# Performance work log

Hardware: AMD Instinct MI355X
Metric: run time of the kernel (lower is better)

Reference implementation:

```python
import jax, jax.numpy as jnp
import numpy as np

D = 512
B = 128
V = 1024
MAX_LEN = 5000


def _pos_encoding(d, max_len):
    # sinusoidal PE table [max_len, d], identical to the torch buffer
    pos = np.arange(max_len, dtype=np.float32)[:, None]
    div = np.exp(np.arange(0, d, 2, dtype=np.float32) * (-np.log(10000.0) / d))
    pe = np.zeros((max_len, d), dtype=np.float32)
    pe[:, 0::2] = np.sin(pos * div)
    pe[:, 1::2] = np.cos(pos * div)
    return jnp.asarray(pe)


def setup_inputs() -> dict:
    key = jax.random.key(0)
    ks = jax.random.split(key, 16)
    s = 0.02  # weight scale
    return {
        "x": jax.random.normal(ks[0], (B, V), jnp.float32),
        "timesteps": jax.random.randint(ks[1], (B,), 0, 1000),
        "query_emb": jax.random.normal(ks[2], (B, D), jnp.float32),
        "target_emb": jax.random.normal(ks[3], (B, V, D), jnp.float32),
        "Wq": jax.random.normal(ks[4], (D, D), jnp.float32) * s,
        "Wk": jax.random.normal(ks[5], (D, D), jnp.float32) * s,
        "Wv": jax.random.normal(ks[6], (D, D), jnp.float32) * s,
        "Wp": jax.random.normal(ks[7], (D, D), jnp.float32) * s,
        "bp": jnp.zeros((D,), jnp.float32),
        "Wt1": jax.random.normal(ks[8], (D, D), jnp.float32) * s,
        "bt1": jnp.zeros((D,), jnp.float32),
        "Wt2": jax.random.normal(ks[9], (D, D), jnp.float32) * s,
        "bt2": jnp.zeros((D,), jnp.float32),
        "Wd1": jax.random.normal(ks[10], (2 * D, 2 * D), jnp.float32) * s,
        "bd1": jnp.zeros((2 * D,), jnp.float32),
        "Wd2": jax.random.normal(ks[11], (1, 2 * D), jnp.float32) * s,
        "bd2": jnp.zeros((1,), jnp.float32),
    }


def reference(x, timesteps, query_emb, target_emb,
              Wq, Wk, Wv, Wp, bp, Wt1, bt1, Wt2, bt2,
              Wd1, bd1, Wd2, bd2):
    pe = _pos_encoding(D, MAX_LEN)
    # timestep embedding: pe[t] -> SiLU MLP  (dropout in eval mode = identity)
    t = pe[timesteps]                                      # [B, D]
    cond = jax.nn.silu(t @ Wt1.T + bt1) @ Wt2.T + bt2      # [B, D]
    q = (query_emb + cond) @ Wq.T                          # [B, D]
    tc = target_emb + cond[:, None, :]                     # [B, V, D]
    k = tc @ Wk.T
    v = tc @ Wv.T
    # single-query attention with additive bias x
    weight = jax.nn.softmax(jnp.einsum('bd,bvd->bv', q, k) + x, axis=-1)  # [B, V]
    new_emb = jnp.einsum('bv,bvd->bd', weight, v) @ Wp.T + bp             # [B, D]
    # concat-MLP decoder over all candidates
    emb = jnp.concatenate(
        [jnp.broadcast_to(new_emb[:, None, :], target_emb.shape), target_emb],
        axis=-1)                                            # [B, V, 2D]
    h = jax.nn.relu(emb @ Wd1.T + bd1)                      # [B, V, 2D]
    p = (h @ Wd2.T + bd2)[..., 0] + weight                  # [B, V]
    return p
```

## Files before the change

### kernel.cpp

```cpp
#include <hip/hip_runtime.h>
#include <hip/hip_bf16.h>


typedef __attribute__((ext_vector_type(8))) short bhalf8_t;
typedef __attribute__((ext_vector_type(8))) unsigned short ushort8_t;
typedef __attribute__((ext_vector_type(4))) float fx4_t;

__device__ __forceinline__ unsigned short f2bf(float f) {
  unsigned int u = __float_as_uint(f);
  unsigned int r = (u + 0x7FFFu + ((u >> 16) & 1u)) >> 16;
  return (unsigned short)r;
}
__device__ __forceinline__ float bf2f(unsigned short h) {
  return __uint_as_float((unsigned int)h << 16);
}

__device__ __forceinline__ float wave_sum64(float s) {
#pragma unroll
  for (int o = 32; o; o >>= 1) s += __shfl_xor(s, o, 64);
  return s;
}

__global__ __launch_bounds__(256) void transpose5_kernel(
    const float* __restrict__ s0, const float* __restrict__ s1, const float* __restrict__ s2,
    const float* __restrict__ s3, const float* __restrict__ s4,
    float* __restrict__ d0, float* __restrict__ d1, float* __restrict__ d2,
    float* __restrict__ d3, float* __restrict__ d4) {
  __shared__ float t[32][33];
  const float* src; float* dst;
  switch (blockIdx.z) {
    case 0: src = s0; dst = d0; break;
    case 1: src = s1; dst = d1; break;
    case 2: src = s2; dst = d2; break;
    case 3: src = s3; dst = d3; break;
    default: src = s4; dst = d4; break;
  }
  const int tx = threadIdx.x & 31, ty = threadIdx.x >> 5;
  const int c0 = blockIdx.x * 32, r0 = blockIdx.y * 32;
#pragma unroll
  for (int i = 0; i < 32; i += 8)
    t[ty + i][tx] = src[(size_t)(r0 + ty + i) * 512 + c0 + tx];
  __syncthreads();
#pragma unroll
  for (int i = 0; i < 32; i += 8)
    dst[(size_t)(c0 + ty + i) * 512 + r0 + tx] = t[tx][ty + i];
}

__global__ __launch_bounds__(256) void transposed1_kernel(const float* __restrict__ src,
                                                          float* __restrict__ dst) {
  __shared__ float t[32][33];
  const int tx = threadIdx.x & 31, ty = threadIdx.x >> 5;
  const int c0 = blockIdx.x * 32, r0 = blockIdx.y * 32;
#pragma unroll
  for (int i = 0; i < 32; i += 8)
    t[ty + i][tx] = src[(size_t)(r0 + ty + i) * 1024 + c0 + tx];
  __syncthreads();
#pragma unroll
  for (int i = 0; i < 32; i += 8)
    dst[(size_t)(c0 + ty + i) * 1024 + r0 + tx] = t[tx][ty + i];
}

template <int MODE, int ACT, int DOT>
__global__ __launch_bounds__(256) void gvec_kernel(
    const float* __restrict__ WT, int n, const float* __restrict__ src1,
    const float* __restrict__ src2, const float* __restrict__ bias,
    const int* __restrict__ timesteps, float* __restrict__ outp,
    float* __restrict__ dotout) {
  __shared__ __attribute__((aligned(16))) float arow[512];
  const int b = blockIdx.x, tid = threadIdx.x;
  if (MODE == 0) {
    const int ts = timesteps[b];
    const float NEG = -9.2103403719761836f / 512.f;
    float dv = expf((float)(2 * tid) * NEG);
    float ang = (float)ts * dv;
    arow[2 * tid] = sinf(ang);
    arow[2 * tid + 1] = cosf(ang);
  } else {
#pragma unroll
    for (int k = tid; k < 512; k += 256) {
      float a;
      if (MODE == 1) {
        a = src1[(size_t)b * 512 + k];
      } else if (MODE == 2) {
        a = src1[(size_t)b * 512 + k] + src2[(size_t)b * 512 + k];
      } else {
        a = src2[(size_t)b * 512 + k];
#pragma unroll
        for (int q = 0; q < 8; ++q) a += src1[((size_t)b * 8 + q) * 512 + k];
      }
      arow[k] = a;
    }
  }
  __syncthreads();
  const int j = blockIdx.y * 256 + tid;
  const float* w = WT + j;
  float s0 = 0.f, s1 = 0.f, s2 = 0.f, s3 = 0.f;
#pragma unroll 4
  for (int k = 0; k < 512; k += 4) {
    s0 = fmaf(arow[k], w[(size_t)k * n], s0);
    s1 = fmaf(arow[k + 1], w[(size_t)(k + 1) * n], s1);
    s2 = fmaf(arow[k + 2], w[(size_t)(k + 2) * n], s2);
    s3 = fmaf(arow[k + 3], w[(size_t)(k + 3) * n], s3);
  }
  float s = (s0 + s1) + (s2 + s3);
  if (bias) s += bias[j];
  if (ACT == 1) s = s / (1.f + expf(-s));
  outp[(size_t)b * n + j] = s;
  if (DOT) {
    float p = s * src2[(size_t)b * 512 + j];
    p = wave_sum64(p);
    __shared__ float rd[4];
    if ((tid & 63) == 0) rd[tid >> 6] = p;
    __syncthreads();
    if (tid == 0) atomicAdd(dotout + b, rd[0] + rd[1] + rd[2] + rd[3]);
  }
}

__global__ __launch_bounds__(256) void convw_kernel(const float* __restrict__ Wd1,
                                                    unsigned short* __restrict__ wsW) {
  const int g = blockIdx.x * 256 + threadIdx.x;
  const int lane = g & 63;
  const int kc = (g >> 6) & 1;
  const int nhn = (g >> 7) & 7;
  const int ks = (g >> 10) & 7;
  const int nc = g >> 13;
  const int j = nc * 128 + (nhn >> 1) * 32 + (nhn & 1) * 16 + (lane & 15);
  const int k = ks * 64 + kc * 32 + (lane >> 4) * 8;
  const float* src = Wd1 + (size_t)j * 1024 + 512 + k;
  float4 f0 = *(const float4*)src;
  float4 f1 = *(const float4*)(src + 4);
  ushort4 h0 = make_ushort4(f2bf(f0.x), f2bf(f0.y), f2bf(f0.z), f2bf(f0.w));
  ushort4 h1 = make_ushort4(f2bf(f1.x), f2bf(f1.y), f2bf(f1.z), f2bf(f1.w));
  ushort4* dst = (ushort4*)((char*)wsW + (size_t)g * 16);
  dst[0] = h0;
  dst[1] = h1;
}

__global__ __launch_bounds__(256) void logits_kernel(
    const float* __restrict__ te, const float* __restrict__ qk,
    const float* __restrict__ constb, const float* __restrict__ x,
    float* __restrict__ logits, unsigned short* __restrict__ te16, int w16) {
  const int wave = threadIdx.x >> 6, lane = threadIdx.x & 63;
  const size_t r = (size_t)blockIdx.x * 4 + wave;
  const int b = (int)(r >> 10);
  const float4* t4 = (const float4*)(te + r * 512);
  const float4* q4 = (const float4*)(qk + (size_t)b * 512);
  float4 a0 = t4[lane], a1 = t4[lane + 64];
  float4 c0 = q4[lane], c1 = q4[lane + 64];
  float s = a0.x * c0.x + a0.y * c0.y + a0.z * c0.z + a0.w * c0.w +
            a1.x * c1.x + a1.y * c1.y + a1.z * c1.z + a1.w * c1.w;
  s = wave_sum64(s);
  if (w16) {
    ushort4 h0 = make_ushort4(f2bf(a0.x), f2bf(a0.y), f2bf(a0.z), f2bf(a0.w));
    ushort4 h1 = make_ushort4(f2bf(a1.x), f2bf(a1.y), f2bf(a1.z), f2bf(a1.w));
    *(ushort4*)(te16 + r * 512 + lane * 4) = h0;
    *(ushort4*)(te16 + r * 512 + 256 + lane * 4) = h1;
  }
  if (lane == 0) logits[r] = s + constb[b] + x[r];
}

__global__ __launch_bounds__(256) void softmax_kernel(
    const float* __restrict__ logits, const float* __restrict__ bd2,
    float* __restrict__ weight, float* __restrict__ out) {
  __shared__ float sm[4];
  const int b = blockIdx.x, tid = threadIdx.x;
  const int wave = tid >> 6, lane = tid & 63;
  float4 l4 = ((const float4*)(logits + (size_t)b * 1024))[tid];
  float m = fmaxf(fmaxf(l4.x, l4.y), fmaxf(l4.z, l4.w));
#pragma unroll
  for (int o = 32; o; o >>= 1) m = fmaxf(m, __shfl_xor(m, o, 64));
  if (lane == 0) sm[wave] = m;
  __syncthreads();
  float M = fmaxf(fmaxf(sm[0], sm[1]), fmaxf(sm[2], sm[3]));
  __syncthreads();
  float e0 = expf(l4.x - M), e1 = expf(l4.y - M), e2 = expf(l4.z - M), e3 = expf(l4.w - M);
  float ssum = wave_sum64(e0 + e1 + e2 + e3);
  if (lane == 0) sm[wave] = ssum;
  __syncthreads();
  float inv = 1.f / (sm[0] + sm[1] + sm[2] + sm[3]);
  float c = bd2[0];
  float4 w4 = make_float4(e0 * inv, e1 * inv, e2 * inv, e3 * inv);
  ((float4*)(weight + (size_t)b * 1024))[tid] = w4;
  ((float4*)(out + (size_t)b * 1024))[tid] = make_float4(w4.x + c, w4.y + c, w4.z + c, w4.w + c);
}

__global__ __launch_bounds__(256) void wsum32_kernel(const float* __restrict__ te,
                                                     const float* __restrict__ weight,
                                                     float* __restrict__ spart) {
  __shared__ float wl[128];
  const int b = blockIdx.x >> 3, vq = blockIdx.x & 7;
  const int tid = threadIdx.x;
  if (tid < 128) wl[tid] = weight[(size_t)b * 1024 + vq * 128 + tid];
  __syncthreads();
  const float* tb = te + ((size_t)b * 1024 + (size_t)vq * 128) * 512;
  float s0 = 0.f, s1 = 0.f;
#pragma unroll 4
  for (int v = 0; v < 128; ++v) {
    float w = wl[v];
    s0 += w * tb[(size_t)v * 512 + tid];
    s1 += w * tb[(size_t)v * 512 + 256 + tid];
  }
  spart[(size_t)blockIdx.x * 512 + tid] = s0;
  spart[(size_t)blockIdx.x * 512 + 256 + tid] = s1;
}

__global__ __launch_bounds__(256) void wsum16_kernel(const unsigned short* __restrict__ te16,
                                                     const float* __restrict__ weight,
                                                     float* __restrict__ spart) {
  __shared__ float wl[128];
  __shared__ float red[4][512];
  const int b = blockIdx.x >> 3, vq = blockIdx.x & 7;
  const int tid = threadIdx.x;
  if (tid < 128) wl[tid] = weight[(size_t)b * 1024 + vq * 128 + tid];
  __syncthreads();
  const int g = tid & 63, vh = tid >> 6;
  const unsigned short* base =
      te16 + ((size_t)b * 1024 + vq * 128 + vh * 32) * 512 + g * 8;
  float acc[8] = {};
  for (int v = 0; v < 32; ++v) {
    float w = wl[vh * 32 + v];
    ushort8_t h = *(const ushort8_t*)(base + (size_t)v * 512);
#pragma unroll
    for (int i = 0; i < 8; ++i) acc[i] += w * bf2f(h[i]);
  }
#pragma unroll
  for (int i = 0; i < 8; ++i) red[vh][g * 8 + i] = acc[i];
  __syncthreads();
  for (int d = tid; d < 512; d += 256)
    spart[(size_t)blockIdx.x * 512 + d] =
        red[0][d] + red[1][d] + red[2][d] + red[3][d];
}

#define GLD16(g, l)                                                              \
  __builtin_amdgcn_global_load_lds((const __attribute__((address_space(1))) void*)(g), \
                                   (__attribute__((address_space(3))) void*)(l), 16, 0, 0)

template <int USE16>
__global__ __launch_bounds__(512, 2) void decoder_kernel(
    const float* __restrict__ te, const unsigned short* __restrict__ te16,
    const unsigned short* __restrict__ wsW, const float* __restrict__ A,
    const float* __restrict__ Wd2, float* __restrict__ out) {
  extern __shared__ char lds[];

  const int tid = threadIdx.x;
  const int wave = tid >> 6, lane = tid & 63;
  const int lhi = lane >> 4, llo = lane & 15;
  const int mh = wave >> 2, nh = wave & 3;
  const size_t row0 = (size_t)blockIdx.x * 64;
  const int b = (int)(blockIdx.x >> 4);

  bhalf8_t a[2][16];
  if (USE16) {
#pragma unroll
    for (int m = 0; m < 2; ++m) {
      const char* rowp = (const char*)te16 + (row0 + mh * 32 + m * 16 + llo) * 1024 + lhi * 16;
#pragma unroll
      for (int s = 0; s < 16; ++s) a[m][s] = *(const bhalf8_t*)(rowp + s * 64);
    }
  } else {
#pragma unroll
    for (int m = 0; m < 2; ++m) {
      const char* rowp = (const char*)te + (row0 + mh * 32 + m * 16 + llo) * 2048 + lhi * 32;
#pragma unroll
      for (int s = 0; s < 16; ++s) {
        float4 f0 = *(const float4*)(rowp + s * 128);
        float4 f1 = *(const float4*)(rowp + s * 128 + 16);
        bhalf8_t h;
        h[0] = (short)f2bf(f0.x); h[1] = (short)f2bf(f0.y);
        h[2] = (short)f2bf(f0.z); h[3] = (short)f2bf(f0.w);
        h[4] = (short)f2bf(f1.x); h[5] = (short)f2bf(f1.y);
        h[6] = (short)f2bf(f1.z); h[7] = (short)f2bf(f1.w);
        a[m][s] = h;
      }
    }
  }

  float av[8][2], wv[8][2];
#pragma unroll
  for (int nc = 0; nc < 8; ++nc) {
    const int jb = nc * 128 + nh * 32 + llo;
    av[nc][0] = A[(size_t)b * 1024 + jb];
    av[nc][1] = A[(size_t)b * 1024 + jb + 16];
    wv[nc][0] = Wd2[jb];
    wv[nc][1] = Wd2[jb + 16];
  }

#pragma unroll
  for (int m = 0; m < 2; ++m)
#pragma unroll
    for (int s = 0; s < 16; ++s) asm volatile("" : "+v"(a[m][s]));
#pragma unroll
  for (int nc = 0; nc < 8; ++nc)
    asm volatile("" : "+v"(av[nc][0]), "+v"(av[nc][1]), "+v"(wv[nc][0]), "+v"(wv[nc][1]));

  auto stage = [&](int c) {
    const char* src = (const char*)wsW + (size_t)c * 16384 + wave * 1024 + lane * 16;
    char* dst = lds + (c & 3) * 16384 + wave * 1024;
    GLD16(src, dst);
    GLD16(src + 8192, dst + 8192);
  };
  stage(0); stage(1); stage(2);

  fx4_t acc[2][2];
  const fx4_t zf = {0.f, 0.f, 0.f, 0.f};
  float pacc[2][4] = {};

#pragma unroll
  for (int nc = 0; nc < 8; ++nc) {
#pragma unroll
    for (int ks = 0; ks < 8; ++ks) {
      const int c = nc * 8 + ks;
      if (c <= 61)      asm volatile("s_waitcnt vmcnt(4)" ::: "memory");
      else if (c == 62) asm volatile("s_waitcnt vmcnt(2)" ::: "memory");
      else              asm volatile("s_waitcnt vmcnt(0)" ::: "memory");
      __builtin_amdgcn_s_barrier();
      __builtin_amdgcn_sched_barrier(0);
      if (ks == 0) { acc[0][0] = zf; acc[0][1] = zf; acc[1][0] = zf; acc[1][1] = zf; }
      const char* wb = lds + (c & 3) * 16384 + nh * 4096 + lane * 16;
      bhalf8_t b00 = *(const bhalf8_t*)(wb);
      bhalf8_t b01 = *(const bhalf8_t*)(wb + 1024);
      bhalf8_t b10 = *(const bhalf8_t*)(wb + 2048);
      bhalf8_t b11 = *(const bhalf8_t*)(wb + 3072);
      acc[0][0] = __builtin_amdgcn_mfma_f32_16x16x32_bf16(a[0][ks * 2 + 0], b00, acc[0][0], 0, 0, 0);
      acc[0][0] = __builtin_amdgcn_mfma_f32_16x16x32_bf16(a[0][ks * 2 + 1], b01, acc[0][0], 0, 0, 0);
      acc[0][1] = __builtin_amdgcn_mfma_f32_16x16x32_bf16(a[0][ks * 2 + 0], b10, acc[0][1], 0, 0, 0);
      acc[0][1] = __builtin_amdgcn_mfma_f32_16x16x32_bf16(a[0][ks * 2 + 1], b11, acc[0][1], 0, 0, 0);
      acc[1][0] = __builtin_amdgcn_mfma_f32_16x16x32_bf16(a[1][ks * 2 + 0], b00, acc[1][0], 0, 0, 0);
      acc[1][0] = __builtin_amdgcn_mfma_f32_16x16x32_bf16(a[1][ks * 2 + 1], b01, acc[1][0], 0, 0, 0);
      acc[1][1] = __builtin_amdgcn_mfma_f32_16x16x32_bf16(a[1][ks * 2 + 0], b10, acc[1][1], 0, 0, 0);
      acc[1][1] = __builtin_amdgcn_mfma_f32_16x16x32_bf16(a[1][ks * 2 + 1], b11, acc[1][1], 0, 0, 0);
      if (c <= 60) stage(c + 3);
      if (ks == 7) {
#pragma unroll
        for (int m = 0; m < 2; ++m)
#pragma unroll
          for (int rg = 0; rg < 4; ++rg)
            pacc[m][rg] += fmaxf(acc[m][0][rg] + av[nc][0], 0.f) * wv[nc][0] +
                           fmaxf(acc[m][1][rg] + av[nc][1], 0.f) * wv[nc][1];
      }
    }
  }

  __syncthreads();
  float* red = (float*)lds;
#pragma unroll
  for (int m = 0; m < 2; ++m)
#pragma unroll
    for (int rg = 0; rg < 4; ++rg) {
      float sv = pacc[m][rg];
      sv += __shfl_xor(sv, 1, 64);
      sv += __shfl_xor(sv, 2, 64);
      sv += __shfl_xor(sv, 4, 64);
      sv += __shfl_xor(sv, 8, 64);
      if (llo == 0) red[nh * 64 + mh * 32 + m * 16 + lhi * 4 + rg] = sv;
    }
  __syncthreads();
  if (tid < 64) {
    float s = red[tid] + red[64 + tid] + red[128 + tid] + red[192 + tid];
    out[row0 + tid] += s;
  }
}

extern "C" void kernel_launch(void* const* d_in, const int* in_sizes, int n_in,
                              void* d_out, int out_size, void* d_ws, size_t ws_size,
                              hipStream_t stream) {
  const float* x = (const float*)d_in[0];
  const int* tsteps = (const int*)d_in[1];
  const float* qe = (const float*)d_in[2];
  const float* te = (const float*)d_in[3];
  const float* Wq = (const float*)d_in[4];
  const float* Wk = (const float*)d_in[5];
  const float* Wv = (const float*)d_in[6];
  const float* Wp = (const float*)d_in[7];
  const float* bp = (const float*)d_in[8];
  const float* Wt1 = (const float*)d_in[9];
  const float* bt1 = (const float*)d_in[10];
  const float* Wt2 = (const float*)d_in[11];
  const float* bt2 = (const float*)d_in[12];
  const float* Wd1 = (const float*)d_in[13];
  const float* bd1 = (const float*)d_in[14];
  const float* Wd2 = (const float*)d_in[15];
  const float* bd2 = (const float*)d_in[16];
  float* out = (float*)d_out;

  char* ws = (char*)d_ws;
  unsigned short* wsW = (unsigned short*)(ws + 0);
  float* Wt1T = (float*)(ws + 1048576);
  float* Wt2T = (float*)(ws + 2097152);
  float* WqT = (float*)(ws + 3145728);
  float* WvT = (float*)(ws + 4194304);
  float* WpT = (float*)(ws + 5242880);
  float* Wd1aT = (float*)(ws + 6291456);
  float* cond = (float*)(ws + 8388608);
  float* qk = (float*)(ws + 8650752);
  float* hbuf = (float*)(ws + 8912896);
  float* qbuf = (float*)(ws + 9175040);
  float* ubuf = (float*)(ws + 9437184);
  float* nebuf = (float*)(ws + 9699328);
  float* cb = (float*)(ws + 9961472);
  float* logits = (float*)(ws + 9965568);
  float* wgt = (float*)(ws + 10489856);
  float* spart = (float*)(ws + 11014144);
  float* Abuf = (float*)(ws + 13111296);
  const size_t TE16_OFF = 14680064;
  const size_t TE16_BYTES = (size_t)128 * 1024 * 512 * 2;
  unsigned short* te16 = (unsigned short*)(ws + TE16_OFF);
  const int use16 = (ws_size >= TE16_OFF + TE16_BYTES) ? 1 : 0;

  transpose5_kernel<<<dim3(16, 16, 5), 256, 0, stream>>>(Wt1, Wt2, Wq, Wv, Wp,
                                                         Wt1T, Wt2T, WqT, WvT, WpT);
  transposed1_kernel<<<dim3(16, 32), 256, 0, stream>>>(Wd1, Wd1aT);
  convw_kernel<<<256, 256, 0, stream>>>(Wd1, wsW);

  hipMemsetAsync(cb, 0, 128 * sizeof(float), stream);
  gvec_kernel<0, 1, 0><<<dim3(128, 2), 256, 0, stream>>>(Wt1T, 512, nullptr, nullptr, bt1, tsteps, hbuf, nullptr);
  gvec_kernel<1, 0, 0><<<dim3(128, 2), 256, 0, stream>>>(Wt2T, 512, hbuf, nullptr, bt2, nullptr, cond, nullptr);
  gvec_kernel<2, 0, 0><<<dim3(128, 2), 256, 0, stream>>>(WqT, 512, qe, cond, nullptr, nullptr, qbuf, nullptr);
  gvec_kernel<1, 0, 1><<<dim3(128, 2), 256, 0, stream>>>(Wk, 512, qbuf, cond, nullptr, nullptr, qk, cb);

  logits_kernel<<<32768, 256, 0, stream>>>(te, qk, cb, x, logits, te16, use16);
  softmax_kernel<<<128, 256, 0, stream>>>(logits, bd2, wgt, out);
  if (use16)
    wsum16_kernel<<<1024, 256, 0, stream>>>(te16, wgt, spart);
  else
    wsum32_kernel<<<1024, 256, 0, stream>>>(te, wgt, spart);

  gvec_kernel<3, 0, 0><<<dim3(128, 2), 256, 0, stream>>>(WvT, 512, spart, cond, nullptr, nullptr, ubuf, nullptr);
  gvec_kernel<1, 0, 0><<<dim3(128, 2), 256, 0, stream>>>(WpT, 512, ubuf, nullptr, bp, nullptr, nebuf, nullptr);
  gvec_kernel<1, 0, 0><<<dim3(128, 4), 256, 0, stream>>>(Wd1aT, 1024, nebuf, nullptr, bd1, nullptr, Abuf, nullptr);

  if (use16) {
    (void)hipFuncSetAttribute((const void*)decoder_kernel<1>,
                              hipFuncAttributeMaxDynamicSharedMemorySize, 65536);
    decoder_kernel<1><<<2048, 512, 65536, stream>>>(te, te16, wsW, Abuf, Wd2, out);
  } else {
    (void)hipFuncSetAttribute((const void*)decoder_kernel<0>,
                              hipFuncAttributeMaxDynamicSharedMemorySize, 65536);
    decoder_kernel<0><<<2048, 512, 65536, stream>>>(te, te16, wsW, Abuf, Wd2, out);
  }
}
```

Baseline: 474.7 us.

## Fuse weight prep and small GEMV chains into few kernels, tweak decoder staging

Merges the transpose and bf16 conversion kernels into one prep launch, fuses the four front GEMVs (timestep MLP, q, qk, cb) into one per-batch kernel, and fuses the three back GEMVs into another. This removes a memset and many small launches along with their intermediate buffers. The decoder now starts weight staging before its A-operand loads, pins the A fragments in AGPRs, drops the occupancy hint from launch bounds, and moves the reduction scratch past a larger LDS allocation. Each fused kernel runs only 128 blocks, so the GEMVs get less parallelism, and the extra LDS may lower decoder occupancy.

```diff
diff --git a/kernel.cpp b/kernel.cpp
--- a/kernel.cpp
+++ b/kernel.cpp
@@ -21,119 +21,199 @@
   return s;
 }
 
-__global__ __launch_bounds__(256) void transpose5_kernel(
-    const float* __restrict__ s0, const float* __restrict__ s1, const float* __restrict__ s2,
-    const float* __restrict__ s3, const float* __restrict__ s4,
-    float* __restrict__ d0, float* __restrict__ d1, float* __restrict__ d2,
-    float* __restrict__ d3, float* __restrict__ d4) {
-  __shared__ float t[32][33];
-  const float* src; float* dst;
-  switch (blockIdx.z) {
-    case 0: src = s0; dst = d0; break;
-    case 1: src = s1; dst = d1; break;
-    case 2: src = s2; dst = d2; break;
-    case 3: src = s3; dst = d3; break;
-    default: src = s4; dst = d4; break;
-  }
-  const int tx = threadIdx.x & 31, ty = threadIdx.x >> 5;
-  const int c0 = blockIdx.x * 32, r0 = blockIdx.y * 32;
-#pragma unroll
-  for (int i = 0; i < 32; i += 8)
-    t[ty + i][tx] = src[(size_t)(r0 + ty + i) * 512 + c0 + tx];
-  __syncthreads();
-#pragma unroll
-  for (int i = 0; i < 32; i += 8)
-    dst[(size_t)(c0 + ty + i) * 512 + r0 + tx] = t[tx][ty + i];
-}
-
-__global__ __launch_bounds__(256) void transposed1_kernel(const float* __restrict__ src,
-                                                          float* __restrict__ dst) {
+__global__ __launch_bounds__(256) void prepw_kernel(
+    const float* __restrict__ Wt1, const float* __restrict__ Wt2, const float* __restrict__ Wq,
+    const float* __restrict__ Wv, const float* __restrict__ Wp, const float* __restrict__ Wd1,
+    float* __restrict__ Wt1T, float* __restrict__ Wt2T, float* __restrict__ WqT,
+    float* __restrict__ WvT, float* __restrict__ WpT, float* __restrict__ Wd1aT,
+    unsigned short* __restrict__ wsW) {
+  const int z = blockIdx.z;
+  if (z == 6) {
+    if (blockIdx.y >= 16) return;
+    const int g = (blockIdx.y * 16 + blockIdx.x) * 256 + threadIdx.x;
+    const int lane = g & 63;
+    const int kc = (g >> 6) & 1;
+    const int nhn = (g >> 7) & 7;
+    const int ks = (g >> 10) & 7;
+    const int nc = g >> 13;
+    const int j = nc * 128 + (nhn >> 1) * 32 + (nhn & 1) * 16 + (lane & 15);
+    const int k = ks * 64 + kc * 32 + (lane >> 4) * 8;
+    const float* src = Wd1 + (size_t)j * 1024 + 512 + k;
+    float4 f0 = *(const float4*)src;
+    float4 f1 = *(const float4*)(src + 4);
+    ushort4 h0 = make_ushort4(f2bf(f0.x), f2bf(f0.y), f2bf(f0.z), f2bf(f0.w));
+    ushort4 h1 = make_ushort4(f2bf(f1.x), f2bf(f1.y), f2bf(f1.z), f2bf(f1.w));
+    ushort4* dst = (ushort4*)((char*)wsW + (size_t)g * 16);
+    dst[0] = h0;
+    dst[1] = h1;
+    return;
+  }
   __shared__ float t[32][33];
   const int tx = threadIdx.x & 31, ty = threadIdx.x >> 5;
   const int c0 = blockIdx.x * 32, r0 = blockIdx.y * 32;
+  if (z == 5) {
+    const float* src = Wd1;
+    float* dst = Wd1aT;
+#pragma unroll
+    for (int i = 0; i < 32; i += 8)
+      t[ty + i][tx] = src[(size_t)(r0 + ty + i) * 1024 + c0 + tx];
+    __syncthreads();
+#pragma unroll
+    for (int i = 0; i < 32; i += 8)
+      dst[(size_t)(c0 + ty + i) * 1024 + r0 + tx] = t[tx][ty + i];
+    return;
+  }
+  if (blockIdx.y >= 16) return;
+  const float* src;
+  float* dst;
+  switch (z) {
+    case 0: src = Wt1; dst = Wt1T; break;
+    case 1: src = Wt2; dst = Wt2T; break;
+    case 2: src = Wq; dst = WqT; break;
+    case 3: src = Wv; dst = WvT; break;
+    default: src = Wp; dst = WpT; break;
+  }
 #pragma unroll
   for (int i = 0; i < 32; i += 8)
-    t[ty + i][tx] = src[(size_t)(r0 + ty + i) * 1024 + c0 + tx];
+    t[ty + i][tx] = src[(size_t)(r0 + ty + i) * 512 + c0 + tx];
   __syncthreads();
 #pragma unroll
   for (int i = 0; i < 32; i += 8)
-    dst[(size_t)(c0 + ty + i) * 1024 + r0 + tx] = t[tx][ty + i];
-}
-
-template <int MODE, int ACT, int DOT>
-__global__ __launch_bounds__(256) void gvec_kernel(
-    const float* __restrict__ WT, int n, const float* __restrict__ src1,
-    const float* __restrict__ src2, const float* __restrict__ bias,
-    const int* __restrict__ timesteps, float* __restrict__ outp,
-    float* __restrict__ dotout) {
-  __shared__ __attribute__((aligned(16))) float arow[512];
+    dst[(size_t)(c0 + ty + i) * 512 + r0 + tx] = t[tx][ty + i];
+}
+
+__global__ __launch_bounds__(512) void front_kernel(
+    const int* __restrict__ timesteps, const float* __restrict__ qe,
+    const float* __restrict__ Wt1T, const float* __restrict__ bt1,
+    const float* __restrict__ Wt2T, const float* __restrict__ bt2,
+    const float* __restrict__ WqT, const float* __restrict__ Wk,
+    float* __restrict__ cond_out, float* __restrict__ qk_out, float* __restrict__ cb_out) {
+  __shared__ __attribute__((aligned(16))) float v0[512], v1[512], v2[512];
+  __shared__ float rd[8];
   const int b = blockIdx.x, tid = threadIdx.x;
-  if (MODE == 0) {
+  if (tid < 256) {
     const int ts = timesteps[b];
     const float NEG = -9.2103403719761836f / 512.f;
     float dv = expf((float)(2 * tid) * NEG);
     float ang = (float)ts * dv;
-    arow[2 * tid] = sinf(ang);
-    arow[2 * tid + 1] = cosf(ang);
-  } else {
-#pragma unroll
-    for (int k = tid; k < 512; k += 256) {
-      float a;
-      if (MODE == 1) {
-        a = src1[(size_t)b * 512 + k];
-      } else if (MODE == 2) {
-        a = src1[(size_t)b * 512 + k] + src2[(size_t)b * 512 + k];
-      } else {
-        a = src2[(size_t)b * 512 + k];
-#pragma unroll
-        for (int q = 0; q < 8; ++q) a += src1[((size_t)b * 8 + q) * 512 + k];
-      }
-      arow[k] = a;
-    }
-  }
-  __syncthreads();
-  const int j = blockIdx.y * 256 + tid;
-  const float* w = WT + j;
-  float s0 = 0.f, s1 = 0.f, s2 = 0.f, s3 = 0.f;
-#pragma unroll 4
-  for (int k = 0; k < 512; k += 4) {
-    s0 = fmaf(arow[k], w[(size_t)k * n], s0);
-    s1 = fmaf(arow[k + 1], w[(size_t)(k + 1) * n], s1);
-    s2 = fmaf(arow[k + 2], w[(size_t)(k + 2) * n], s2);
-    s3 = fmaf(arow[k + 3], w[(size_t)(k + 3) * n], s3);
-  }
-  float s = (s0 + s1) + (s2 + s3);
-  if (bias) s += bias[j];
-  if (ACT == 1) s = s / (1.f + expf(-s));
-  outp[(size_t)b * n + j] = s;
-  if (DOT) {
-    float p = s * src2[(size_t)b * 512 + j];
-    p = wave_sum64(p);
-    __shared__ float rd[4];
+    v0[2 * tid] = sinf(ang);
+    v0[2 * tid + 1] = cosf(ang);
+  }
+  __syncthreads();
+  {
+    float s0 = 0.f, s1 = 0.f, s2 = 0.f, s3 = 0.f;
+#pragma unroll 4
+    for (int k = 0; k < 512; k += 4) {
+      s0 = fmaf(v0[k], Wt1T[(size_t)k * 512 + tid], s0);
+      s1 = fmaf(v0[k + 1], Wt1T[(size_t)(k + 1) * 512 + tid], s1);
+      s2 = fmaf(v0[k + 2], Wt1T[(size_t)(k + 2) * 512 + tid], s2);
+      s3 = fmaf(v0[k + 3], Wt1T[(size_t)(k + 3) * 512 + tid], s3);
+    }
+    float s = (s0 + s1) + (s2 + s3) + bt1[tid];
+    s = s / (1.f + expf(-s));
+    v1[tid] = s;
+  }
+  __syncthreads();
+  {
+    float s0 = 0.f, s1 = 0.f, s2 = 0.f, s3 = 0.f;
+#pragma unroll 4
+    for (int k = 0; k < 512; k += 4) {
+      s0 = fmaf(v1[k], Wt2T[(size_t)k * 512 + tid], s0);
+      s1 = fmaf(v1[k + 1], Wt2T[(size_t)(k + 1) * 512 + tid], s1);
+      s2 = fmaf(v1[k + 2], Wt2T[(size_t)(k + 2) * 512 + tid], s2);
+      s3 = fmaf(v1[k + 3], Wt2T[(size_t)(k + 3) * 512 + tid], s3);
+    }
+    float s = (s0 + s1) + (s2 + s3) + bt2[tid];
+    v0[tid] = s;
+    cond_out[(size_t)b * 512 + tid] = s;
+    v1[tid] = qe[(size_t)b * 512 + tid] + s;
+  }
+  __syncthreads();
+  {
+    float s0 = 0.f, s1 = 0.f, s2 = 0.f, s3 = 0.f;
+#pragma unroll 4
+    for (int k = 0; k < 512; k += 4) {
+      s0 = fmaf(v1[k], WqT[(size_t)k * 512 + tid], s0);
+      s1 = fmaf(v1[k + 1], WqT[(size_t)(k + 1) * 512 + tid], s1);
+      s2 = fmaf(v1[k + 2], WqT[(size_t)(k + 2) * 512 + tid], s2);
+      s3 = fmaf(v1[k + 3], WqT[(size_t)(k + 3) * 512 + tid], s3);
+    }
+    v2[tid] = (s0 + s1) + (s2 + s3);
+  }
+  __syncthreads();
+  {
+    float s0 = 0.f, s1 = 0.f, s2 = 0.f, s3 = 0.f;
+#pragma unroll 4
+    for (int d = 0; d < 512; d += 4) {
+      s0 = fmaf(v2[d], Wk[(size_t)d * 512 + tid], s0);
+      s1 = fmaf(v2[d + 1], Wk[(size_t)(d + 1) * 512 + tid], s1);
+      s2 = fmaf(v2[d + 2], Wk[(size_t)(d + 2) * 512 + tid], s2);
+      s3 = fmaf(v2[d + 3], Wk[(size_t)(d + 3) * 512 + tid], s3);
+    }
+    float qkv = (s0 + s1) + (s2 + s3);
+    qk_out[(size_t)b * 512 + tid] = qkv;
+    float p = wave_sum64(qkv * v0[tid]);
     if ((tid & 63) == 0) rd[tid >> 6] = p;
-    __syncthreads();
-    if (tid == 0) atomicAdd(dotout + b, rd[0] + rd[1] + rd[2] + rd[3]);
-  }
-}
-
-__global__ __launch_bounds__(256) void convw_kernel(const float* __restrict__ Wd1,
-                                                    unsigned short* __restrict__ wsW) {
-  const int g = blockIdx.x * 256 + threadIdx.x;
-  const int lane = g & 63;
-  const int kc = (g >> 6) & 1;
-  const int nhn = (g >> 7) & 7;
-  const int ks = (g >> 10) & 7;
-  const int nc = g >> 13;
-  const int j = nc * 128 + (nhn >> 1) * 32 + (nhn & 1) * 16 + (lane & 15);
-  const int k = ks * 64 + kc * 32 + (lane >> 4) * 8;
-  const float* src = Wd1 + (size_t)j * 1024 + 512 + k;
-  float4 f0 = *(const float4*)src;
-  float4 f1 = *(const float4*)(src + 4);
-  ushort4 h0 = make_ushort4(f2bf(f0.x), f2bf(f0.y), f2bf(f0.z), f2bf(f0.w));
-  ushort4 h1 = make_ushort4(f2bf(f1.x), f2bf(f1.y), f2bf(f1.z), f2bf(f1.w));
-  ushort4* dst = (ushort4*)((char*)wsW + (size_t)g * 16);
-  dst[0] = h0;
-  dst[1] = h1;
+  }
+  __syncthreads();
+  if (tid == 0) {
+    float c = 0.f;
+#pragma unroll
+    for (int w = 0; w < 8; ++w) c += rd[w];
+    cb_out[b] = c;
+  }
+}
+
+__global__ __launch_bounds__(512) void back_kernel(
+    const float* __restrict__ spart, const float* __restrict__ cond,
+    const float* __restrict__ WvT, const float* __restrict__ WpT, const float* __restrict__ bp,
+    const float* __restrict__ Wd1aT, const float* __restrict__ bd1, float* __restrict__ Abuf) {
+  __shared__ __attribute__((aligned(16))) float v0[512], v1[512];
+  const int b = blockIdx.x, tid = threadIdx.x;
+  {
+    float s = cond[(size_t)b * 512 + tid];
+#pragma unroll
+    for (int q = 0; q < 8; ++q) s += spart[((size_t)b * 8 + q) * 512 + tid];
+    v0[tid] = s;
+  }
+  __syncthreads();
+  {
+    float s0 = 0.f, s1 = 0.f, s2 = 0.f, s3 = 0.f;
+#pragma unroll 4
+    for (int k = 0; k < 512; k += 4) {
+      s0 = fmaf(v0[k], WvT[(size_t)k * 512 + tid], s0);
+      s1 = fmaf(v0[k + 1], WvT[(size_t)(k + 1) * 512 + tid], s1);
+      s2 = fmaf(v0[k + 2], WvT[(size_t)(k + 2) * 512 + tid], s2);
+      s3 = fmaf(v0[k + 3], WvT[(size_t)(k + 3) * 512 + tid], s3);
+    }
+    v1[tid] = (s0 + s1) + (s2 + s3);
+  }
+  __syncthreads();
+  {
+    float s0 = 0.f, s1 = 0.f, s2 = 0.f, s3 = 0.f;
+#pragma unroll 4
+    for (int k = 0; k < 512; k += 4) {
+      s0 = fmaf(v1[k], WpT[(size_t)k * 512 + tid], s0);
+      s1 = fmaf(v1[k + 1], WpT[(size_t)(k + 1) * 512 + tid], s1);
+      s2 = fmaf(v1[k + 2], WpT[(size_t)(k + 2) * 512 + tid], s2);
+      s3 = fmaf(v1[k + 3], WpT[(size_t)(k + 3) * 512 + tid], s3);
+    }
+    v0[tid] = (s0 + s1) + (s2 + s3) + bp[tid];
+  }
+  __syncthreads();
+  {
+    float a0 = 0.f, a1 = 0.f, b0 = 0.f, b1 = 0.f;
+#pragma unroll 2
+    for (int k = 0; k < 512; k += 2) {
+      float x0 = v0[k], x1 = v0[k + 1];
+      a0 = fmaf(x0, Wd1aT[(size_t)k * 1024 + tid], a0);
+      a1 = fmaf(x1, Wd1aT[(size_t)(k + 1) * 1024 + tid], a1);
+      b0 = fmaf(x0, Wd1aT[(size_t)k * 1024 + 512 + tid], b0);
+      b1 = fmaf(x1, Wd1aT[(size_t)(k + 1) * 1024 + 512 + tid], b1);
+    }
+    Abuf[(size_t)b * 1024 + tid] = a0 + a1 + bd1[tid];
+    Abuf[(size_t)b * 1024 + 512 + tid] = b0 + b1 + bd1[512 + tid];
+  }
 }
 
 __global__ __launch_bounds__(256) void logits_kernel(
@@ -236,11 +316,12 @@
                                    (__attribute__((address_space(3))) void*)(l), 16, 0, 0)
 
 template <int USE16>
-__global__ __launch_bounds__(512, 2) void decoder_kernel(
+__global__ __launch_bounds__(512) void decoder_kernel(
     const float* __restrict__ te, const unsigned short* __restrict__ te16,
     const unsigned short* __restrict__ wsW, const float* __restrict__ A,
     const float* __restrict__ Wd2, float* __restrict__ out) {
   extern __shared__ char lds[];
+  char* ring = lds;
 
   const int tid = threadIdx.x;
   const int wave = tid >> 6, lane = tid & 63;
@@ -248,6 +329,14 @@
   const int mh = wave >> 2, nh = wave & 3;
   const size_t row0 = (size_t)blockIdx.x * 64;
   const int b = (int)(blockIdx.x >> 4);
+
+  auto stage = [&](int c) {
+    const char* src = (const char*)wsW + (size_t)c * 16384 + wave * 1024 + lane * 16;
+    char* dst = ring + (c & 3) * 16384 + wave * 1024;
+    GLD16(src, dst);
+    GLD16(src + 8192, dst + 8192);
+  };
+  stage(0); stage(1); stage(2);
 
   bhalf8_t a[2][16];
   if (USE16) {
@@ -276,30 +365,27 @@
   }
 
   float av[8][2], wv[8][2];
-#pragma unroll
-  for (int nc = 0; nc < 8; ++nc) {
-    const int jb = nc * 128 + nh * 32 + llo;
-    av[nc][0] = A[(size_t)b * 1024 + jb];
-    av[nc][1] = A[(size_t)b * 1024 + jb + 16];
-    wv[nc][0] = Wd2[jb];
-    wv[nc][1] = Wd2[jb + 16];
+  {
+    const float* A_g = A + (size_t)b * 1024;
+#pragma unroll
+    for (int nc = 0; nc < 8; ++nc) {
+      const int jb = nc * 128 + nh * 32 + llo;
+      av[nc][0] = A_g[jb];
+      av[nc][1] = A_g[jb + 16];
+      wv[nc][0] = Wd2[jb];
+      wv[nc][1] = Wd2[jb + 16];
+    }
   }
 
 #pragma unroll
   for (int m = 0; m < 2; ++m)
 #pragma unroll
-    for (int s = 0; s < 16; ++s) asm volatile("" : "+v"(a[m][s]));
+    for (int s = 0; s < 16; ++s) asm volatile("" : "+a"(a[m][s]));
 #pragma unroll
   for (int nc = 0; nc < 8; ++nc)
     asm volatile("" : "+v"(av[nc][0]), "+v"(av[nc][1]), "+v"(wv[nc][0]), "+v"(wv[nc][1]));
 
-  auto stage = [&](int c) {
-    const char* src = (const char*)wsW + (size_t)c * 16384 + wave * 1024 + lane * 16;
-    char* dst = lds + (c & 3) * 16384 + wave * 1024;
-    GLD16(src, dst);
-    GLD16(src + 8192, dst + 8192);
-  };
-  stage(0); stage(1); stage(2);
+  __syncthreads();
 
   fx4_t acc[2][2];
   const fx4_t zf = {0.f, 0.f, 0.f, 0.f};
@@ -316,7 +402,7 @@
       __builtin_amdgcn_s_barrier();
       __builtin_amdgcn_sched_barrier(0);
       if (ks == 0) { acc[0][0] = zf; acc[0][1] = zf; acc[1][0] = zf; acc[1][1] = zf; }
-      const char* wb = lds + (c & 3) * 16384 + nh * 4096 + lane * 16;
+      const char* wb = ring + (c & 3) * 16384 + nh * 4096 + lane * 16;
       bhalf8_t b00 = *(const bhalf8_t*)(wb);
       bhalf8_t b01 = *(const bhalf8_t*)(wb + 1024);
       bhalf8_t b10 = *(const bhalf8_t*)(wb + 2048);
@@ -332,17 +418,18 @@
       if (c <= 60) stage(c + 3);
       if (ks == 7) {
 #pragma unroll
-        for (int m = 0; m < 2; ++m)
-#pragma unroll
-          for (int rg = 0; rg < 4; ++rg)
-            pacc[m][rg] += fmaxf(acc[m][0][rg] + av[nc][0], 0.f) * wv[nc][0] +
-                           fmaxf(acc[m][1][rg] + av[nc][1], 0.f) * wv[nc][1];
+        for (int n = 0; n < 2; ++n)
+#pragma unroll
+          for (int m = 0; m < 2; ++m)
+#pragma unroll
+            for (int rg = 0; rg < 4; ++rg)
+              pacc[m][rg] += fmaxf(acc[m][n][rg] + av[nc][n], 0.f) * wv[nc][n];
       }
     }
   }
 
   __syncthreads();
-  float* red = (float*)lds;
+  float* red = (float*)(lds + 65536);
 #pragma unroll
   for (int m = 0; m < 2; ++m)
 #pragma unroll
@@ -393,10 +480,6 @@
   float* Wd1aT = (float*)(ws + 6291456);
   float* cond = (float*)(ws + 8388608);
   float* qk = (float*)(ws + 8650752);
-  float* hbuf = (float*)(ws + 8912896);
-  float* qbuf = (float*)(ws + 9175040);
-  float* ubuf = (float*)(ws + 9437184);
-  float* nebuf = (float*)(ws + 9699328);
   float* cb = (float*)(ws + 9961472);
   float* logits = (float*)(ws + 9965568);
   float* wgt = (float*)(ws + 10489856);
@@ -407,35 +490,24 @@
   unsigned short* te16 = (unsigned short*)(ws + TE16_OFF);
   const int use16 = (ws_size >= TE16_OFF + TE16_BYTES) ? 1 : 0;
 
-  transpose5_kernel<<<dim3(16, 16, 5), 256, 0, stream>>>(Wt1, Wt2, Wq, Wv, Wp,
-                                                         Wt1T, Wt2T, WqT, WvT, WpT);
-  transposed1_kernel<<<dim3(16, 32), 256, 0, stream>>>(Wd1, Wd1aT);
-  convw_kernel<<<256, 256, 0, stream>>>(Wd1, wsW);
-
-  hipMemsetAsync(cb, 0, 128 * sizeof(float), stream);
-  gvec_kernel<0, 1, 0><<<dim3(128, 2), 256, 0, stream>>>(Wt1T, 512, nullptr, nullptr, bt1, tsteps, hbuf, nullptr);
-  gvec_kernel<1, 0, 0><<<dim3(128, 2), 256, 0, stream>>>(Wt2T, 512, hbuf, nullptr, bt2, nullptr, cond, nullptr);
-  gvec_kernel<2, 0, 0><<<dim3(128, 2), 256, 0, stream>>>(WqT, 512, qe, cond, nullptr, nullptr, qbuf, nullptr);
-  gvec_kernel<1, 0, 1><<<dim3(128, 2), 256, 0, stream>>>(Wk, 512, qbuf, cond, nullptr, nullptr, qk, cb);
-
+  prepw_kernel<<<dim3(16, 32, 7), 256, 0, stream>>>(Wt1, Wt2, Wq, Wv, Wp, Wd1,
+                                                    Wt1T, Wt2T, WqT, WvT, WpT, Wd1aT, wsW);
+  front_kernel<<<128, 512, 0, stream>>>(tsteps, qe, Wt1T, bt1, Wt2T, bt2, WqT, Wk,
+                                        cond, qk, cb);
   logits_kernel<<<32768, 256, 0, stream>>>(te, qk, cb, x, logits, te16, use16);
   softmax_kernel<<<128, 256, 0, stream>>>(logits, bd2, wgt, out);
   if (use16)
     wsum16_kernel<<<1024, 256, 0, stream>>>(te16, wgt, spart);
   else
     wsum32_kernel<<<1024, 256, 0, stream>>>(te, wgt, spart);
-
-  gvec_kernel<3, 0, 0><<<dim3(128, 2), 256, 0, stream>>>(WvT, 512, spart, cond, nullptr, nullptr, ubuf, nullptr);
-  gvec_kernel<1, 0, 0><<<dim3(128, 2), 256, 0, stream>>>(WpT, 512, ubuf, nullptr, bp, nullptr, nebuf, nullptr);
-  gvec_kernel<1, 0, 0><<<dim3(128, 4), 256, 0, stream>>>(Wd1aT, 1024, nebuf, nullptr, bd1, nullptr, Abuf, nullptr);
-
+  back_kernel<<<128, 512, 0, stream>>>(spart, cond, WvT, WpT, bp, Wd1aT, bd1, Abuf);
   if (use16) {
     (void)hipFuncSetAttribute((const void*)decoder_kernel<1>,
-                              hipFuncAttributeMaxDynamicSharedMemorySize, 65536);
-    decoder_kernel<1><<<2048, 512, 65536, stream>>>(te, te16, wsW, Abuf, Wd2, out);
+                              hipFuncAttributeMaxDynamicSharedMemorySize, 67584);
+    decoder_kernel<1><<<2048, 512, 67584, stream>>>(te, te16, wsW, Abuf, Wd2, out);
   } else {
     (void)hipFuncSetAttribute((const void*)decoder_kernel<0>,
-                              hipFuncAttributeMaxDynamicSharedMemorySize, 65536);
-    decoder_kernel<0><<<2048, 512, 65536, stream>>>(te, te16, wsW, Abuf, Wd2, out);
-  }
-}
+                              hipFuncAttributeMaxDynamicSharedMemorySize, 67584);
+    decoder_kernel<0><<<2048, 512, 67584, stream>>>(te, te16, wsW, Abuf, Wd2, out);
+  }
+}
```

Measured after the change: 566.1 us. +19.2%, slower.
